# Optimization experiments

Hardware: AMD Instinct MI355X
Metric: run time of the kernel (lower is better)

Reference implementation:

```python
import jax, jax.numpy as jnp
import numpy as np

BRANCH, VOCAB, FFN, BATCH = 8, 256, 1024, 16384
LN_EPS = 1e-5


def setup_inputs() -> dict:
    key = jax.random.key(0)
    ks = jax.random.split(key, 7)
    x = jax.random.normal(ks[0], (BATCH, BRANCH, VOCAB), dtype=jnp.float32)
    U1 = 0.01 * jax.random.normal(ks[1], (BRANCH, VOCAB, FFN), dtype=jnp.float32)
    b1 = 0.01 * jax.random.normal(ks[2], (BRANCH, FFN), dtype=jnp.float32)
    U2 = 0.01 * jax.random.normal(ks[3], (BRANCH, FFN, VOCAB), dtype=jnp.float32)
    b2 = 0.01 * jax.random.normal(ks[4], (BRANCH, VOCAB), dtype=jnp.float32)
    ln_w = jnp.ones((VOCAB,), dtype=jnp.float32)
    ln_b = jnp.zeros((VOCAB,), dtype=jnp.float32)
    return {"x": x, "U1": U1, "b1": b1, "U2": U2, "b2": b2, "ln_w": ln_w, "ln_b": ln_b}


def _layernorm(h, w, b):
    mu = jnp.mean(h, axis=-1, keepdims=True)
    var = jnp.var(h, axis=-1, keepdims=True)
    return (h - mu) * jax.lax.rsqrt(var + LN_EPS) * w + b


def reference(x, U1, b1, U2, b2, ln_w, ln_b):
    # x: (B, N, D); branch-wise batched GEMMs via einsum (avoids explicit permutes)
    skip = x
    h = jnp.einsum('bnd,nde->bne', x, U1) + b1        # (B, N, FFN)
    h = jax.nn.gelu(h, approximate=False)
    h = jnp.einsum('bne,ned->bnd', h, U2) + b2        # (B, N, VOCAB)
    h = _layernorm(h, ln_w, ln_b)
    h = jax.nn.gelu(h, approximate=False)
    out = skip + h
    return out.reshape(BATCH, 1, BRANCH * VOCAB)
```

## Files before the change

kernel.cpp:

```cpp
#include <hip/hip_runtime.h>
#include <hip/hip_bf16.h>

#define B_TOT 16384
#define NBR   8
#define DV    256
#define FF    1024
#define ROWS  128
#define FC    64
#define NCHUNK 16

using bf16x8 = __attribute__((ext_vector_type(8))) short;
using f32x4  = __attribute__((ext_vector_type(4))) float;

__device__ __forceinline__ unsigned short f2bf(float f) {
    unsigned int u = __builtin_bit_cast(unsigned int, f);
    unsigned int r = (u + 0x7fffu + ((u >> 16) & 1u)) >> 16;
    return (unsigned short)r;
}
__device__ __forceinline__ float bf2f(unsigned short h) {
    unsigned int u = ((unsigned int)h) << 16;
    return __builtin_bit_cast(float, u);
}
__device__ __forceinline__ float gelu_fast(float x) {
    float x2 = x * x;
    float z  = x * fmaf(x2, -0.1029434959f, -2.3022078770f);
    float e  = __builtin_amdgcn_exp2f(z);
    return x * __builtin_amdgcn_rcpf(1.0f + e);
}

#define GLL(gsrc, ldst) __builtin_amdgcn_global_load_lds((const unsigned int*)(gsrc), (unsigned int*)(ldst), 16, 0, 0)

__global__ void prep_weights(const float* __restrict__ U1, const float* __restrict__ U2,
                             unsigned short* __restrict__ w1img, unsigned short* __restrict__ w2img)
{
    const int b = blockIdx.x;
    const int n = b >> 4, c = b & 15;
    const int tid = threadIdx.x;
    char* img1 = (char*)(w1img) + ((size_t)b << 15);
    char* img2 = (char*)(w2img) + ((size_t)b << 15);
    const float* U1n = U1 + (size_t)n * DV * FF;
    const float* U2n = U2 + (size_t)n * FF * DV;
    #pragma unroll 4
    for (int e = 0; e < 64; ++e) {
        int kk = e * 4 + (tid >> 6);
        int nn = tid & 63;
        float v = U1n[(size_t)kk * FF + c * 64 + nn];
        unsigned off = ((unsigned)(nn * 256 + kk) * 2u) ^ (unsigned)((nn & 7) << 4);
        *(unsigned short*)(img1 + off) = f2bf(v);
    }
    #pragma unroll 4
    for (int e = 0; e < 64; ++e) {
        int nn = tid;
        float v = U2n[(size_t)(c * 64 + e) * DV + nn];
        unsigned off = ((unsigned)(nn * 64 + e) * 2u) ^ (unsigned)((nn & 7) << 4);
        *(unsigned short*)(img2 + off) = f2bf(v);
    }
}

struct alignas(16) Lds {
    char xs[65536];
    char b1[32768];
    char b2[32768];
    char hs[16384];
};

__global__ __launch_bounds__(512, 2)
void belayer_main(const float* __restrict__ x,
                  const unsigned short* __restrict__ w1img,
                  const unsigned short* __restrict__ w2img,
                  const float* __restrict__ b1, const float* __restrict__ b2,
                  const float* __restrict__ lnw, const float* __restrict__ lnb,
                  float* __restrict__ out)
{
    __shared__ Lds S;
    const int tid  = threadIdx.x;
    const int lane = tid & 63;
    const int wave = tid >> 6;
    const int n    = blockIdx.x & 7;
    const int tile = blockIdx.x >> 3;
    const int row0 = tile * ROWS;

    #pragma unroll
    for (int p = 0; p < 8; ++p) {
        int r  = (tid >> 5) + p * 16;
        int kc = (tid & 31) * 8;
        const float* src = x + ((size_t)(row0 + r) * NBR + n) * DV + kc;
        f32x4 v0 = *(const f32x4*)src;
        f32x4 v1 = *(const f32x4*)(src + 4);
        bf16x8 h;
        h[0] = (short)f2bf(v0[0]); h[1] = (short)f2bf(v0[1]);
        h[2] = (short)f2bf(v0[2]); h[3] = (short)f2bf(v0[3]);
        h[4] = (short)f2bf(v1[0]); h[5] = (short)f2bf(v1[1]);
        h[6] = (short)f2bf(v1[2]); h[7] = (short)f2bf(v1[3]);
        *(bf16x8*)(S.xs + (((r * 256 + kc) * 2) ^ ((r & 7) << 4))) = h;
    }
    {
        const char* g = (const char*)w1img + ((size_t)(n * 16) << 15) + (wave << 12) + lane * 16;
        char* l = S.b1 + (wave << 12);
        #pragma unroll
        for (int i = 0; i < 4; ++i) GLL(g + (i << 10), l + (i << 10));
    }
    __syncthreads();

    const int rowgrp = wave >> 1;
    const int colsel = wave & 1;
    bf16x8 A[2][8];
    #pragma unroll
    for (int rf = 0; rf < 2; ++rf)
        #pragma unroll
        for (int ks = 0; ks < 8; ++ks) {
            int rr = rowgrp * 32 + rf * 16 + (lane & 15);
            int kk = ks * 32 + (lane >> 4) * 8;
            A[rf][ks] = *(const bf16x8*)(S.xs + (((rr * 256 + kk) * 2) ^ ((rr & 7) << 4)));
        }

    const int rowg2 = wave >> 2;
    const int colg2 = wave & 3;
    f32x4 acc2[4][4];
    #pragma unroll
    for (int i = 0; i < 4; ++i)
        #pragma unroll
        for (int j = 0; j < 4; ++j) acc2[i][j] = (f32x4){0.f, 0.f, 0.f, 0.f};

    for (int c = 0; c < NCHUNK; ++c) {
        {
            const char* g = (const char*)w2img + ((size_t)(n * 16 + c) << 15) + (wave << 12) + lane * 16;
            char* l = S.b2 + (wave << 12);
            #pragma unroll
            for (int i = 0; i < 4; ++i) GLL(g + (i << 10), l + (i << 10));
        }
        f32x4 acc1[2][2];
        #pragma unroll
        for (int i = 0; i < 2; ++i)
            #pragma unroll
            for (int j = 0; j < 2; ++j) acc1[i][j] = (f32x4){0.f, 0.f, 0.f, 0.f};
        #pragma unroll
        for (int ks = 0; ks < 8; ++ks) {
            int kk = ks * 32 + (lane >> 4) * 8;
            int nn0 = colsel * 32 + (lane & 15);
            int nn1 = nn0 + 16;
            bf16x8 bf0 = *(const bf16x8*)(S.b1 + (((nn0 * 256 + kk) * 2) ^ ((nn0 & 7) << 4)));
            bf16x8 bf1 = *(const bf16x8*)(S.b1 + (((nn1 * 256 + kk) * 2) ^ ((nn1 & 7) << 4)));
            acc1[0][0] = __builtin_amdgcn_mfma_f32_16x16x32_bf16(A[0][ks], bf0, acc1[0][0], 0, 0, 0);
            acc1[0][1] = __builtin_amdgcn_mfma_f32_16x16x32_bf16(A[0][ks], bf1, acc1[0][1], 0, 0, 0);
            acc1[1][0] = __builtin_amdgcn_mfma_f32_16x16x32_bf16(A[1][ks], bf0, acc1[1][0], 0, 0, 0);
            acc1[1][1] = __builtin_amdgcn_mfma_f32_16x16x32_bf16(A[1][ks], bf1, acc1[1][1], 0, 0, 0);
        }
        #pragma unroll
        for (int cf = 0; cf < 2; ++cf) {
            int hk = colsel * 32 + cf * 16 + (lane & 15);
            float b1v = b1[n * FF + c * 64 + hk];
            #pragma unroll
            for (int rf = 0; rf < 2; ++rf)
                #pragma unroll
                for (int r = 0; r < 4; ++r) {
                    int row = rowgrp * 32 + rf * 16 + (lane >> 4) * 4 + r;
                    float g = gelu_fast(acc1[rf][cf][r] + b1v);
                    *(unsigned short*)(S.hs + (((row * 64 + hk) * 2) ^ ((row & 7) << 4))) = f2bf(g);
                }
        }
        __syncthreads();

        if (c < NCHUNK - 1) {
            const char* g = (const char*)w1img + ((size_t)(n * 16 + c + 1) << 15) + (wave << 12) + lane * 16;
            char* l = S.b1 + (wave << 12);
            #pragma unroll
            for (int i = 0; i < 4; ++i) GLL(g + (i << 10), l + (i << 10));
        }
        #pragma unroll
        for (int ks = 0; ks < 2; ++ks) {
            int kb = ks * 32 + (lane >> 4) * 8;
            bf16x8 af[4], bfr[4];
            #pragma unroll
            for (int rf = 0; rf < 4; ++rf) {
                int rr = rowg2 * 64 + rf * 16 + (lane & 15);
                af[rf] = *(const bf16x8*)(S.hs + (((rr * 64 + kb) * 2) ^ ((rr & 7) << 4)));
            }
            #pragma unroll
            for (int cf = 0; cf < 4; ++cf) {
                int nn = colg2 * 64 + cf * 16 + (lane & 15);
                bfr[cf] = *(const bf16x8*)(S.b2 + (((nn * 64 + kb) * 2) ^ ((nn & 7) << 4)));
            }
            #pragma unroll
            for (int rf = 0; rf < 4; ++rf)
                #pragma unroll
                for (int cf = 0; cf < 4; ++cf)
                    acc2[rf][cf] = __builtin_amdgcn_mfma_f32_16x16x32_bf16(af[rf], bfr[cf], acc2[rf][cf], 0, 0, 0);
        }
        __syncthreads();
    }

    float b2v[4];
    #pragma unroll
    for (int cf = 0; cf < 4; ++cf) b2v[cf] = b2[n * DV + colg2 * 64 + cf * 16 + (lane & 15)];

    float sA[4][4], sQ[4][4];
    #pragma unroll
    for (int rf = 0; rf < 4; ++rf)
        #pragma unroll
        for (int r = 0; r < 4; ++r) { sA[rf][r] = 0.f; sQ[rf][r] = 0.f; }
    #pragma unroll
    for (int rf = 0; rf < 4; ++rf)
        #pragma unroll
        for (int cf = 0; cf < 4; ++cf)
            #pragma unroll
            for (int r = 0; r < 4; ++r) {
                float v = acc2[rf][cf][r] + b2v[cf];
                acc2[rf][cf][r] = v;
                sA[rf][r] += v;
                sQ[rf][r] += v * v;
            }
    #pragma unroll
    for (int m = 1; m < 16; m <<= 1)
        #pragma unroll
        for (int rf = 0; rf < 4; ++rf)
            #pragma unroll
            for (int r = 0; r < 4; ++r) {
                sA[rf][r] += __shfl_xor(sA[rf][r], m, 64);
                sQ[rf][r] += __shfl_xor(sQ[rf][r], m, 64);
            }
    float* Lred = (float*)S.hs;
    if ((lane & 15) == 0) {
        #pragma unroll
        for (int rf = 0; rf < 4; ++rf)
            #pragma unroll
            for (int r = 0; r < 4; ++r) {
                int row = rowg2 * 64 + rf * 16 + (lane >> 4) * 4 + r;
                Lred[colg2 * 128 + row]       = sA[rf][r];
                Lred[512 + colg2 * 128 + row] = sQ[rf][r];
            }
    }
    __syncthreads();
    float mu[4][4], rs[4][4];
    #pragma unroll
    for (int rf = 0; rf < 4; ++rf)
        #pragma unroll
        for (int r = 0; r < 4; ++r) {
            int row = rowg2 * 64 + rf * 16 + (lane >> 4) * 4 + r;
            float ssum = Lred[row] + Lred[128 + row] + Lred[256 + row] + Lred[384 + row];
            float qsum = Lred[512 + row] + Lred[640 + row] + Lred[768 + row] + Lred[896 + row];
            float m_ = ssum * (1.0f / 256.0f);
            float var = qsum * (1.0f / 256.0f) - m_ * m_;
            mu[rf][r] = m_;
            rs[rf][r] = rsqrtf(var + 1e-5f);
        }
    #pragma unroll
    for (int cf = 0; cf < 4; ++cf) {
        int col = colg2 * 64 + cf * 16 + (lane & 15);
        float lw = lnw[col];
        float lb = lnb[col];
        #pragma unroll
        for (int rf = 0; rf < 4; ++rf)
            #pragma unroll
            for (int r = 0; r < 4; ++r) {
                int row = rowg2 * 64 + rf * 16 + (lane >> 4) * 4 + r;
                float v = (acc2[rf][cf][r] - mu[rf][r]) * rs[rf][r] * lw + lb;
                float g = gelu_fast(v);
                unsigned short sk = *(const unsigned short*)(S.xs + (((row * 256 + col) * 2) ^ ((row & 7) << 4)));
                out[((size_t)(row0 + row) * NBR + n) * DV + col] = bf2f(sk) + g;
            }
    }
}

extern "C" void kernel_launch(void* const* d_in, const int* in_sizes, int n_in,
                              void* d_out, int out_size, void* d_ws, size_t ws_size,
                              hipStream_t stream) {
    const float* x   = (const float*)d_in[0];
    const float* U1  = (const float*)d_in[1];
    const float* b1  = (const float*)d_in[2];
    const float* U2  = (const float*)d_in[3];
    const float* b2  = (const float*)d_in[4];
    const float* lnw = (const float*)d_in[5];
    const float* lnb = (const float*)d_in[6];
    float* out = (float*)d_out;

    unsigned short* w1img = (unsigned short*)d_ws;
    unsigned short* w2img = w1img + (size_t)4 * 1024 * 1024 / 2;

    prep_weights<<<dim3(128), dim3(256), 0, stream>>>(U1, U2, w1img, w2img);
    belayer_main<<<dim3(1024), dim3(512), 0, stream>>>(x, w1img, w2img, b1, b2, lnw, lnb, out);
}
```

Before: 270.3 us.

## Double-buffer weight and hidden tiles, software-pipeline GEMM2 behind GEMM1, drop x staging

Removes the 64KB bf16 x staging buffer in LDS. x is loaded straight from global into A-fragment registers, and the skip values are re-read in fp32 from global during the epilogue, so the residual is now added at full precision. The freed LDS double-buffers the W1, W2 and hidden tiles, so each chunk's GEMM2 runs one iteration behind GEMM1 and weight prefetches overlap compute. Full __syncthreads is replaced by partial vmcnt waits plus raw barriers, and LDS addresses are precomputed. This adds register pressure from the extra skip registers and relies on hand-tuned waitcnt ordering being correct.

```diff
diff --git a/kernel.cpp b/kernel.cpp
--- a/kernel.cpp
+++ b/kernel.cpp
@@ -1,13 +1,16 @@
 #include <hip/hip_runtime.h>
 #include <hip/hip_bf16.h>
 
-#define B_TOT 16384
 #define NBR   8
 #define DV    256
 #define FF    1024
 #define ROWS  128
-#define FC    64
 #define NCHUNK 16
+
+#define L_B1 0
+#define L_B2 65536
+#define L_HS 131072
+#define LDS_BYTES 163840
 
 using bf16x8 = __attribute__((ext_vector_type(8))) short;
 using f32x4  = __attribute__((ext_vector_type(4))) float;
@@ -29,12 +32,13 @@
 }
 
 #define GLL(gsrc, ldst) __builtin_amdgcn_global_load_lds((const unsigned int*)(gsrc), (unsigned int*)(ldst), 16, 0, 0)
+#define MFMA16 __builtin_amdgcn_mfma_f32_16x16x32_bf16
 
 __global__ void prep_weights(const float* __restrict__ U1, const float* __restrict__ U2,
                              unsigned short* __restrict__ w1img, unsigned short* __restrict__ w2img)
 {
     const int b = blockIdx.x;
-    const int n = b >> 4, c = b & 15;
+    const int n = b >> 4, cch = b & 15;
     const int tid = threadIdx.x;
     char* img1 = (char*)(w1img) + ((size_t)b << 15);
     char* img2 = (char*)(w2img) + ((size_t)b << 15);
@@ -44,155 +48,180 @@
     for (int e = 0; e < 64; ++e) {
         int kk = e * 4 + (tid >> 6);
         int nn = tid & 63;
-        float v = U1n[(size_t)kk * FF + c * 64 + nn];
+        float v = U1n[(size_t)kk * FF + cch * 64 + nn];
         unsigned off = ((unsigned)(nn * 256 + kk) * 2u) ^ (unsigned)((nn & 7) << 4);
         *(unsigned short*)(img1 + off) = f2bf(v);
     }
     #pragma unroll 4
     for (int e = 0; e < 64; ++e) {
         int nn = tid;
-        float v = U2n[(size_t)(c * 64 + e) * DV + nn];
+        float v = U2n[(size_t)(cch * 64 + e) * DV + nn];
         unsigned off = ((unsigned)(nn * 64 + e) * 2u) ^ (unsigned)((nn & 7) << 4);
         *(unsigned short*)(img2 + off) = f2bf(v);
     }
 }
-
-struct alignas(16) Lds {
-    char xs[65536];
-    char b1[32768];
-    char b2[32768];
-    char hs[16384];
-};
 
 __global__ __launch_bounds__(512, 2)
 void belayer_main(const float* __restrict__ x,
                   const unsigned short* __restrict__ w1img,
                   const unsigned short* __restrict__ w2img,
-                  const float* __restrict__ b1, const float* __restrict__ b2,
+                  const float* __restrict__ b1g, const float* __restrict__ b2g,
                   const float* __restrict__ lnw, const float* __restrict__ lnb,
                   float* __restrict__ out)
 {
-    __shared__ Lds S;
+    __shared__ __align__(16) char LDS[LDS_BYTES];
     const int tid  = threadIdx.x;
     const int lane = tid & 63;
     const int wave = tid >> 6;
+    const int q = lane >> 4, c = lane & 15;
     const int n    = blockIdx.x & 7;
     const int tile = blockIdx.x >> 3;
     const int row0 = tile * ROWS;
-
-    #pragma unroll
-    for (int p = 0; p < 8; ++p) {
-        int r  = (tid >> 5) + p * 16;
-        int kc = (tid & 31) * 8;
-        const float* src = x + ((size_t)(row0 + r) * NBR + n) * DV + kc;
-        f32x4 v0 = *(const f32x4*)src;
-        f32x4 v1 = *(const f32x4*)(src + 4);
-        bf16x8 h;
-        h[0] = (short)f2bf(v0[0]); h[1] = (short)f2bf(v0[1]);
-        h[2] = (short)f2bf(v0[2]); h[3] = (short)f2bf(v0[3]);
-        h[4] = (short)f2bf(v1[0]); h[5] = (short)f2bf(v1[1]);
-        h[6] = (short)f2bf(v1[2]); h[7] = (short)f2bf(v1[3]);
-        *(bf16x8*)(S.xs + (((r * 256 + kc) * 2) ^ ((r & 7) << 4))) = h;
-    }
-    {
-        const char* g = (const char*)w1img + ((size_t)(n * 16) << 15) + (wave << 12) + lane * 16;
-        char* l = S.b1 + (wave << 12);
-        #pragma unroll
-        for (int i = 0; i < 4; ++i) GLL(g + (i << 10), l + (i << 10));
-    }
-    __syncthreads();
-
-    const int rowgrp = wave >> 1;
-    const int colsel = wave & 1;
+    const int rowgrp = wave >> 1, colsel = wave & 1;
+    const int rowg2  = wave >> 2, colg2  = wave & 3;
+    const unsigned swz = (unsigned)((c & 7) << 4);
+
+    const char* g1base = (const char*)w1img + ((size_t)(n * 16) << 15) + (wave << 12) + lane * 16;
+    const char* g2base = (const char*)w2img + ((size_t)(n * 16) << 15) + (wave << 12) + lane * 16;
+
+    #pragma unroll
+    for (int i = 0; i < 4; ++i) GLL(g1base + (i << 10), LDS + L_B1 + (wave << 12) + (i << 10));
+    #pragma unroll
+    for (int i = 0; i < 4; ++i) GLL(g2base + (i << 10), LDS + L_B2 + (wave << 12) + (i << 10));
+
     bf16x8 A[2][8];
     #pragma unroll
-    for (int rf = 0; rf < 2; ++rf)
+    for (int rf = 0; rf < 2; ++rf) {
+        const float* src = x + (((size_t)(row0 + rowgrp * 32 + rf * 16 + c)) * NBR + n) * DV + q * 8;
         #pragma unroll
         for (int ks = 0; ks < 8; ++ks) {
-            int rr = rowgrp * 32 + rf * 16 + (lane & 15);
-            int kk = ks * 32 + (lane >> 4) * 8;
-            A[rf][ks] = *(const bf16x8*)(S.xs + (((rr * 256 + kk) * 2) ^ ((rr & 7) << 4)));
-        }
-
-    const int rowg2 = wave >> 2;
-    const int colg2 = wave & 3;
+            f32x4 v0 = *(const f32x4*)(src + ks * 32);
+            f32x4 v1 = *(const f32x4*)(src + ks * 32 + 4);
+            bf16x8 h;
+            h[0] = (short)f2bf(v0[0]); h[1] = (short)f2bf(v0[1]);
+            h[2] = (short)f2bf(v0[2]); h[3] = (short)f2bf(v0[3]);
+            h[4] = (short)f2bf(v1[0]); h[5] = (short)f2bf(v1[1]);
+            h[6] = (short)f2bf(v1[2]); h[7] = (short)f2bf(v1[3]);
+            A[rf][ks] = h;
+        }
+    }
+
+    const unsigned nn01 = (unsigned)(colsel * 32 + c);
+    const unsigned aB1e = (nn01 * 512 + q * 16) ^ swz;
+    const unsigned aB1o = (nn01 * 512 + q * 16 + 64) ^ swz;
+    const unsigned rr0  = (unsigned)(rowg2 * 64 + c);
+    const unsigned aHe  = (rr0 * 128 + q * 16) ^ swz;
+    const unsigned aHo  = (rr0 * 128 + q * 16 + 64) ^ swz;
+    const unsigned nn02 = (unsigned)(colg2 * 64 + c);
+    const unsigned aB2e = (nn02 * 128 + q * 16) ^ swz;
+    const unsigned aB2o = (nn02 * 128 + q * 16 + 64) ^ swz;
+    unsigned aW[4][2];
+    #pragma unroll
+    for (int r = 0; r < 4; ++r)
+        #pragma unroll
+        for (int cf = 0; cf < 2; ++cf)
+            aW[r][cf] = (unsigned)(((rowgrp * 32 + q * 4 + r) * 128 + (colsel * 32 + cf * 16 + c) * 2)
+                                   ^ ((((q & 1) * 4 + r)) << 4));
+
     f32x4 acc2[4][4];
     #pragma unroll
     for (int i = 0; i < 4; ++i)
         #pragma unroll
         for (int j = 0; j < 4; ++j) acc2[i][j] = (f32x4){0.f, 0.f, 0.f, 0.f};
 
-    for (int c = 0; c < NCHUNK; ++c) {
+    asm volatile("s_waitcnt vmcnt(0)" ::: "memory");
+    __builtin_amdgcn_s_barrier();
+    asm volatile("" ::: "memory");
+
+#define G2_PHASE(TPREV)                                                                     \
+    {                                                                                       \
+        const unsigned hOff  = L_HS + ((((TPREV) & 1)) << 14);                              \
+        const unsigned b2Off = L_B2 + ((((TPREV) & 1)) << 15);                              \
+        _Pragma("unroll")                                                                   \
+        for (int ks = 0; ks < 2; ++ks) {                                                    \
+            const unsigned hb = (ks ? aHo : aHe) + hOff;                                    \
+            const unsigned bb = (ks ? aB2o : aB2e) + b2Off;                                 \
+            bf16x8 af[4], bfr[4];                                                           \
+            _Pragma("unroll")                                                               \
+            for (int rf = 0; rf < 4; ++rf) af[rf]  = *(const bf16x8*)(LDS + hb + rf * 2048);\
+            _Pragma("unroll")                                                               \
+            for (int cf = 0; cf < 4; ++cf) bfr[cf] = *(const bf16x8*)(LDS + bb + cf * 2048);\
+            _Pragma("unroll")                                                               \
+            for (int rf = 0; rf < 4; ++rf)                                                  \
+                _Pragma("unroll")                                                           \
+                for (int cf = 0; cf < 4; ++cf)                                              \
+                    acc2[rf][cf] = MFMA16(af[rf], bfr[cf], acc2[rf][cf], 0, 0, 0);          \
+        }                                                                                   \
+    }
+
+    #pragma unroll 2
+    for (int t = 0; t < NCHUNK; ++t) {
+        const int tsrc = (t < NCHUNK - 1) ? (t + 1) : (NCHUNK - 1);
         {
-            const char* g = (const char*)w2img + ((size_t)(n * 16 + c) << 15) + (wave << 12) + lane * 16;
-            char* l = S.b2 + (wave << 12);
+            const char* g = g1base + ((size_t)tsrc << 15);
+            char* l = LDS + L_B1 + (((t + 1) & 1) << 15) + (wave << 12);
             #pragma unroll
             for (int i = 0; i < 4; ++i) GLL(g + (i << 10), l + (i << 10));
         }
-        f32x4 acc1[2][2];
-        #pragma unroll
-        for (int i = 0; i < 2; ++i)
-            #pragma unroll
-            for (int j = 0; j < 2; ++j) acc1[i][j] = (f32x4){0.f, 0.f, 0.f, 0.f};
-        #pragma unroll
-        for (int ks = 0; ks < 8; ++ks) {
-            int kk = ks * 32 + (lane >> 4) * 8;
-            int nn0 = colsel * 32 + (lane & 15);
-            int nn1 = nn0 + 16;
-            bf16x8 bf0 = *(const bf16x8*)(S.b1 + (((nn0 * 256 + kk) * 2) ^ ((nn0 & 7) << 4)));
-            bf16x8 bf1 = *(const bf16x8*)(S.b1 + (((nn1 * 256 + kk) * 2) ^ ((nn1 & 7) << 4)));
-            acc1[0][0] = __builtin_amdgcn_mfma_f32_16x16x32_bf16(A[0][ks], bf0, acc1[0][0], 0, 0, 0);
-            acc1[0][1] = __builtin_amdgcn_mfma_f32_16x16x32_bf16(A[0][ks], bf1, acc1[0][1], 0, 0, 0);
-            acc1[1][0] = __builtin_amdgcn_mfma_f32_16x16x32_bf16(A[1][ks], bf0, acc1[1][0], 0, 0, 0);
-            acc1[1][1] = __builtin_amdgcn_mfma_f32_16x16x32_bf16(A[1][ks], bf1, acc1[1][1], 0, 0, 0);
-        }
-        #pragma unroll
-        for (int cf = 0; cf < 2; ++cf) {
-            int hk = colsel * 32 + cf * 16 + (lane & 15);
-            float b1v = b1[n * FF + c * 64 + hk];
-            #pragma unroll
-            for (int rf = 0; rf < 2; ++rf)
+        if (t >= 1) G2_PHASE(t - 1)
+        asm volatile("s_waitcnt vmcnt(8)\n\ts_waitcnt lgkmcnt(0)" ::: "memory");
+        __builtin_amdgcn_s_barrier();
+        asm volatile("" ::: "memory");
+        {
+            const char* g = g2base + ((size_t)tsrc << 15);
+            char* l = LDS + L_B2 + (((t + 1) & 1) << 15) + (wave << 12);
+            #pragma unroll
+            for (int i = 0; i < 4; ++i) GLL(g + (i << 10), l + (i << 10));
+        }
+        {
+            const unsigned b1Off = L_B1 + ((t & 1) << 15);
+            f32x4 acc1[2][2];
+            #pragma unroll
+            for (int i = 0; i < 2; ++i)
                 #pragma unroll
-                for (int r = 0; r < 4; ++r) {
-                    int row = rowgrp * 32 + rf * 16 + (lane >> 4) * 4 + r;
-                    float g = gelu_fast(acc1[rf][cf][r] + b1v);
-                    *(unsigned short*)(S.hs + (((row * 64 + hk) * 2) ^ ((row & 7) << 4))) = f2bf(g);
-                }
-        }
-        __syncthreads();
-
-        if (c < NCHUNK - 1) {
-            const char* g = (const char*)w1img + ((size_t)(n * 16 + c + 1) << 15) + (wave << 12) + lane * 16;
-            char* l = S.b1 + (wave << 12);
-            #pragma unroll
-            for (int i = 0; i < 4; ++i) GLL(g + (i << 10), l + (i << 10));
-        }
-        #pragma unroll
-        for (int ks = 0; ks < 2; ++ks) {
-            int kb = ks * 32 + (lane >> 4) * 8;
-            bf16x8 af[4], bfr[4];
-            #pragma unroll
-            for (int rf = 0; rf < 4; ++rf) {
-                int rr = rowg2 * 64 + rf * 16 + (lane & 15);
-                af[rf] = *(const bf16x8*)(S.hs + (((rr * 64 + kb) * 2) ^ ((rr & 7) << 4)));
-            }
-            #pragma unroll
-            for (int cf = 0; cf < 4; ++cf) {
-                int nn = colg2 * 64 + cf * 16 + (lane & 15);
-                bfr[cf] = *(const bf16x8*)(S.b2 + (((nn * 64 + kb) * 2) ^ ((nn & 7) << 4)));
-            }
-            #pragma unroll
-            for (int rf = 0; rf < 4; ++rf)
+                for (int j = 0; j < 2; ++j) acc1[i][j] = (f32x4){0.f, 0.f, 0.f, 0.f};
+            #pragma unroll
+            for (int ks = 0; ks < 8; ++ks) {
+                const unsigned bb = ((ks & 1) ? aB1o : aB1e) + b1Off + (ks >> 1) * 128;
+                bf16x8 b0 = *(const bf16x8*)(LDS + bb);
+                bf16x8 b1 = *(const bf16x8*)(LDS + bb + 8192);
+                acc1[0][0] = MFMA16(A[0][ks], b0, acc1[0][0], 0, 0, 0);
+                acc1[0][1] = MFMA16(A[0][ks], b1, acc1[0][1], 0, 0, 0);
+                acc1[1][0] = MFMA16(A[1][ks], b0, acc1[1][0], 0, 0, 0);
+                acc1[1][1] = MFMA16(A[1][ks], b1, acc1[1][1], 0, 0, 0);
+            }
+            const unsigned hw = L_HS + ((t & 1) << 14);
+            #pragma unroll
+            for (int cf = 0; cf < 2; ++cf) {
+                float b1v = b1g[n * FF + t * 64 + colsel * 32 + cf * 16 + c];
                 #pragma unroll
-                for (int cf = 0; cf < 4; ++cf)
-                    acc2[rf][cf] = __builtin_amdgcn_mfma_f32_16x16x32_bf16(af[rf], bfr[cf], acc2[rf][cf], 0, 0, 0);
-        }
-        __syncthreads();
-    }
-
+                for (int rf = 0; rf < 2; ++rf)
+                    #pragma unroll
+                    for (int r = 0; r < 4; ++r) {
+                        float g = gelu_fast(acc1[rf][cf][r] + b1v);
+                        *(unsigned short*)(LDS + hw + aW[r][cf] + rf * 2048) = f2bf(g);
+                    }
+            }
+        }
+        asm volatile("s_waitcnt vmcnt(8)\n\ts_waitcnt lgkmcnt(0)" ::: "memory");
+        __builtin_amdgcn_s_barrier();
+        asm volatile("" ::: "memory");
+    }
+    G2_PHASE(NCHUNK - 1)
+
+    float skp[4][4][4];
+    #pragma unroll
+    for (int rf = 0; rf < 4; ++rf)
+        #pragma unroll
+        for (int r = 0; r < 4; ++r) {
+            const float* xr = x + ((size_t)(row0 + rowg2 * 64 + rf * 16 + q * 4 + r) * NBR + n) * DV;
+            #pragma unroll
+            for (int cf = 0; cf < 4; ++cf)
+                skp[rf][cf][r] = xr[colg2 * 64 + cf * 16 + c];
+        }
     float b2v[4];
     #pragma unroll
-    for (int cf = 0; cf < 4; ++cf) b2v[cf] = b2[n * DV + colg2 * 64 + cf * 16 + (lane & 15)];
+    for (int cf = 0; cf < 4; ++cf) b2v[cf] = b2g[n * DV + colg2 * 64 + cf * 16 + c];
 
     float sA[4][4], sQ[4][4];
     #pragma unroll
@@ -219,13 +248,13 @@
                 sA[rf][r] += __shfl_xor(sA[rf][r], m, 64);
                 sQ[rf][r] += __shfl_xor(sQ[rf][r], m, 64);
             }
-    float* Lred = (float*)S.hs;
-    if ((lane & 15) == 0) {
+    float* Lred = (float*)(LDS + L_HS);
+    if (c == 0) {
         #pragma unroll
         for (int rf = 0; rf < 4; ++rf)
             #pragma unroll
             for (int r = 0; r < 4; ++r) {
-                int row = rowg2 * 64 + rf * 16 + (lane >> 4) * 4 + r;
+                int row = rowg2 * 64 + rf * 16 + q * 4 + r;
                 Lred[colg2 * 128 + row]       = sA[rf][r];
                 Lred[512 + colg2 * 128 + row] = sQ[rf][r];
             }
@@ -236,7 +265,7 @@
     for (int rf = 0; rf < 4; ++rf)
         #pragma unroll
         for (int r = 0; r < 4; ++r) {
-            int row = rowg2 * 64 + rf * 16 + (lane >> 4) * 4 + r;
+            int row = rowg2 * 64 + rf * 16 + q * 4 + r;
             float ssum = Lred[row] + Lred[128 + row] + Lred[256 + row] + Lred[384 + row];
             float qsum = Lred[512 + row] + Lred[640 + row] + Lred[768 + row] + Lred[896 + row];
             float m_ = ssum * (1.0f / 256.0f);
@@ -246,20 +275,20 @@
         }
     #pragma unroll
     for (int cf = 0; cf < 4; ++cf) {
-        int col = colg2 * 64 + cf * 16 + (lane & 15);
+        int col = colg2 * 64 + cf * 16 + c;
         float lw = lnw[col];
         float lb = lnb[col];
         #pragma unroll
         for (int rf = 0; rf < 4; ++rf)
             #pragma unroll
             for (int r = 0; r < 4; ++r) {
-                int row = rowg2 * 64 + rf * 16 + (lane >> 4) * 4 + r;
+                int row = rowg2 * 64 + rf * 16 + q * 4 + r;
                 float v = (acc2[rf][cf][r] - mu[rf][r]) * rs[rf][r] * lw + lb;
                 float g = gelu_fast(v);
-                unsigned short sk = *(const unsigned short*)(S.xs + (((row * 256 + col) * 2) ^ ((row & 7) << 4)));
-                out[((size_t)(row0 + row) * NBR + n) * DV + col] = bf2f(sk) + g;
-            }
-    }
+                out[((size_t)(row0 + row) * NBR + n) * DV + col] = skp[rf][cf][r] + g;
+            }
+    }
+#undef G2_PHASE
 }
 
 extern "C" void kernel_launch(void* const* d_in, const int* in_sizes, int n_in,
```

Result: no change. 275.5 us (+1.9%).
